# Kernel tuning notes

Hardware: AMD Instinct MI355X
Metric: run time of the kernel (lower is better)

## Reference

```python
import jax, jax.numpy as jnp
import numpy as np

B, S, D, H = 4, 2048, 1024, 16
HD = D // H

def setup_inputs() -> dict:
    key = jax.random.key(0)
    ks = jax.random.split(key, 5)
    scale = 1.0 / np.sqrt(D)
    x = jax.random.normal(ks[0], (B, S, D), dtype=jnp.float32)
    Wq = jax.random.uniform(ks[1], (D, D), dtype=jnp.float32, minval=-scale, maxval=scale)
    Wk = jax.random.uniform(ks[2], (D, D), dtype=jnp.float32, minval=-scale, maxval=scale)
    Wv = jax.random.uniform(ks[3], (D, D), dtype=jnp.float32, minval=-scale, maxval=scale)
    Wo = jax.random.uniform(ks[4], (D, D), dtype=jnp.float32, minval=-scale, maxval=scale)
    return {"x": x, "Wq": Wq, "Wk": Wk, "Wv": Wv, "Wo": Wo}

def reference(x, Wq, Wk, Wv, Wo):
    # q/k/v: [B,S,D] @ [D,D] -> [B,S,H,HD] -> [B,H,S,HD]
    def heads(w):
        return (x @ w.T).reshape(B, S, H, HD).transpose(0, 2, 1, 3)
    q, k, v = heads(Wq), heads(Wk), heads(Wv)
    scores = jnp.einsum('bhqd,bhkd->bhqk', q, k) / np.sqrt(HD).astype(x.dtype)
    attn = jax.nn.softmax(scores, axis=-1)  # [B,H,S,S]
    out = jnp.einsum('bhqk,bhkd->bhqd', attn, v)
    out = out.transpose(0, 2, 1, 3).reshape(B, S, D)
    return out @ Wo.T
```

## Files before the change

### kernel.cpp

```cpp
#include <hip/hip_runtime.h>

typedef unsigned short u16;
typedef unsigned int u32;
typedef __attribute__((ext_vector_type(8))) __bf16 bf16x8;
typedef __attribute__((ext_vector_type(4))) float f32x4;

#define B_  4
#define S_  2048
#define D_  1024
#define H_  16
#define HD_ 64

#define MFMA __builtin_amdgcn_mfma_f32_16x16x32_bf16


__device__ __forceinline__ u16 f2bf(float f) {
  union { float f; u32 u; } v; v.f = f;
  u32 r = v.u + 0x7fffu + ((v.u >> 16) & 1u);
  return (u16)(r >> 16);
}

__device__ __forceinline__ void gld16(const void* g, void* l) {
  __builtin_amdgcn_global_load_lds((__attribute__((address_space(1))) void*)g,
                                   (__attribute__((address_space(3))) void*)l,
                                   16, 0, 0);
}

__device__ __forceinline__ u32 pack_bf(float lo, float hi) {
  u32 a = __builtin_bit_cast(u32, lo) + 0x8000u;
  u32 b = __builtin_bit_cast(u32, hi) + 0x8000u;
  return __builtin_amdgcn_perm(b, a, 0x07060302u);
}

__global__ __launch_bounds__(256) void cvt_kernel(const float* __restrict__ src,
                                                  u16* __restrict__ dst, int n) {
  int i = (blockIdx.x * 256 + threadIdx.x) * 4;
  if (i + 3 < n) {
    float4 v = *(const float4*)(src + i);
    ushort4 o;
    o.x = f2bf(v.x); o.y = f2bf(v.y); o.z = f2bf(v.z); o.w = f2bf(v.w);
    *(ushort4*)(dst + i) = o;
  }
}

__global__ __launch_bounds__(256) void cvt4_kernel(const float* __restrict__ s0,
                                                   const float* __restrict__ s1,
                                                   const float* __restrict__ s2,
                                                   const float* __restrict__ s3,
                                                   u16* __restrict__ dst) {
  const float* srcs[4] = {s0, s1, s2, s3};
  const float* src = srcs[blockIdx.y];
  u16* d = dst + (size_t)blockIdx.y * (D_ * D_);
  int i = (blockIdx.x * 256 + threadIdx.x) * 4;
  float4 v = *(const float4*)(src + i);
  ushort4 o;
  o.x = f2bf(v.x); o.y = f2bf(v.y); o.z = f2bf(v.z); o.w = f2bf(v.w);
  *(ushort4*)(d + i) = o;
}

__global__ __launch_bounds__(256) void gemm_bt(const u16* __restrict__ A,
                                               const u16* __restrict__ Bm,
                                               u16* __restrict__ Qfp,
                                               u16* __restrict__ Kfp,
                                               u16* __restrict__ Vfp,
                                               float* __restrict__ f32Out,
                                               int mode) {
  __shared__ u16 As[128 * 32];
  __shared__ u16 Bs[128 * 32];
  const int t = threadIdx.x, w = t >> 6, l = t & 63;
  const int lrow = l & 15, quad = l >> 4;
  const int wr = w >> 1, wc = w & 1;
  const int r0 = blockIdx.y * 128, c0 = blockIdx.x * 128;
  const int srow = l >> 2, scol = (l & 3) * 8;

  f32x4 acc[4][4] = {};

  for (int k0 = 0; k0 < 1024; k0 += 32) {
#pragma unroll
    for (int j = 0; j < 2; j++) {
      int rowA = 32 * w + 16 * j + srow;
      gld16(A + (size_t)(r0 + rowA) * 1024 + k0 + scol, &As[(32 * w + 16 * j) * 32]);
      gld16(Bm + (size_t)(c0 + rowA) * 1024 + k0 + scol, &Bs[(32 * w + 16 * j) * 32]);
    }
    __syncthreads();

    bf16x8 af[4], bfr[4];
#pragma unroll
    for (int i = 0; i < 4; i++)
      af[i] = *(const bf16x8*)&As[(64 * wr + 16 * i + lrow) * 32 + 8 * quad];
#pragma unroll
    for (int j = 0; j < 4; j++)
      bfr[j] = *(const bf16x8*)&Bs[(64 * wc + 16 * j + lrow) * 32 + 8 * quad];
#pragma unroll
    for (int i = 0; i < 4; i++)
#pragma unroll
      for (int j = 0; j < 4; j++)
        acc[i][j] = MFMA(af[i], bfr[j], acc[i][j], 0, 0, 0);
    __syncthreads();
  }

  if (mode == 1) {
#pragma unroll
    for (int i = 0; i < 4; i++)
#pragma unroll
      for (int j = 0; j < 4; j++)
#pragma unroll
        for (int rr = 0; rr < 4; rr++) {
          int row = r0 + 64 * wr + 16 * i + 4 * quad + rr;
          int col = c0 + 64 * wc + 16 * j + lrow;
          f32Out[(size_t)row * 1024 + col] = acc[i][j][rr];
        }
    return;
  }

  const int mat = c0 >> 10;
  const int hh = ((c0 & 1023) >> 6) + wc;
  const int bb = r0 >> 11;
  const int S0 = (r0 & 2047) + 64 * wr;
  u16* hb = (mat == 0 ? Qfp : (mat == 1 ? Kfp : Vfp)) +
            (size_t)(bb * 16 + hh) * 131072;

  if (mat < 2) {
    const int c_l = quad * 32 + (lrow & 7);
    const int R16 = S0 >> 4;
#pragma unroll
    for (int i = 0; i < 4; i++)
#pragma unroll
      for (int j = 0; j < 4; j++) {
        int oj = (j >> 1) * 512 + ((2 * j + (lrow >> 3)) & 3) * 128;
        u16* p = hb + (R16 + i) * 1024 + oj + c_l;
#pragma unroll
        for (int rr = 0; rr < 4; rr++) p[rr * 8] = f2bf(acc[i][j][rr]);
      }
  } else {
#pragma unroll
    for (int i = 0; i < 4; i++) {
      int blkr = ((S0 >> 5) + ((4 * i + quad) >> 3)) * 4;
      int lanew = (lrow + 16 * ((2 * i + (quad >> 1)) & 3)) * 8 + 4 * (quad & 1);
#pragma unroll
      for (int j = 0; j < 4; j++) {
        uint2 pw;
        pw.x = pack_bf(acc[i][j][0], acc[i][j][1]);
        pw.y = pack_bf(acc[i][j][2], acc[i][j][3]);
        *(uint2*)(hb + (blkr + j) * 512 + lanew) = pw;
      }
    }
  }
}

__global__ __launch_bounds__(256) void attn_kernel(const u16* __restrict__ Qf,
                                                   const u16* __restrict__ Kf,
                                                   const u16* __restrict__ Vf,
                                                   u16* __restrict__ attnb) {
  __shared__ uint2 Ps[4][2][4][16][4];
  const int t = threadIdx.x, w = t >> 6, l = t & 63;
  const int lrow = l & 15, quad = l >> 4;
  const int f = blockIdx.x;
  const int bh = (f & 7) * 8 + (f >> 7);
  const int qb0 = (f >> 3) & 15;
  const int b = bh >> 4, h = bh & 15;
  const int q0 = qb0 * 128;
  const float C = 0.18033688011f;

  const u16* Qh = Qf + (size_t)bh * 131072;
  const u16* kp = Kf + (size_t)bh * 131072 + l * 8;
  const u16* vp = Vf + (size_t)bh * 131072 + l * 8;

  bf16x8 aq[2][2];
#pragma unroll
  for (int g = 0; g < 2; g++) {
    int qb = qb0 * 8 + 2 * w + g;
#pragma unroll
    for (int st = 0; st < 2; st++)
      aq[g][st] = *(const bf16x8*)(Qh + (qb * 2 + st) * 512 + l * 8);
  }

  float lsum[2] = {0.f, 0.f};
  f32x4 acc[2][4] = {};

  for (int kt = 0; kt < S_ / 64; kt++) {
    bf16x8 kf[2][4], vf[2][4];
#pragma unroll
    for (int st = 0; st < 2; st++)
#pragma unroll
      for (int nb = 0; nb < 4; nb++)
        kf[st][nb] = *(const bf16x8*)(kp + (nb * 2 + st) * 512);
#pragma unroll
    for (int st = 0; st < 2; st++)
#pragma unroll
      for (int nb = 0; nb < 4; nb++)
        vf[st][nb] = *(const bf16x8*)(vp + (st * 4 + nb) * 512);
    kp += 4096;
    vp += 4096;

    f32x4 sc[2][4] = {};
#pragma unroll
    for (int st = 0; st < 2; st++)
#pragma unroll
      for (int nb = 0; nb < 4; nb++) {
        sc[0][nb] = MFMA(kf[st][nb], aq[0][st], sc[0][nb], 0, 0, 0);
        sc[1][nb] = MFMA(kf[st][nb], aq[1][st], sc[1][nb], 0, 0, 0);
      }

#pragma unroll
    for (int g = 0; g < 2; g++)
#pragma unroll
      for (int nb = 0; nb < 4; nb++) {
        float p0 = __builtin_amdgcn_exp2f(sc[g][nb][0] * C);
        float p1 = __builtin_amdgcn_exp2f(sc[g][nb][1] * C);
        float p2 = __builtin_amdgcn_exp2f(sc[g][nb][2] * C);
        float p3 = __builtin_amdgcn_exp2f(sc[g][nb][3] * C);
        lsum[g] += (p0 + p1) + (p2 + p3);
        uint2 pw;
        pw.x = pack_bf(p0, p1);
        pw.y = pack_bf(p2, p3);
        Ps[w][g][nb][lrow][quad] = pw;
      }

    bf16x8 pf[2][2];
#pragma unroll
    for (int g = 0; g < 2; g++)
#pragma unroll
      for (int st = 0; st < 2; st++)
        pf[g][st] = *(const bf16x8*)&Ps[w][g][2 * st + (quad >> 1)][lrow][2 * (quad & 1)];

#pragma unroll
    for (int st = 0; st < 2; st++)
#pragma unroll
      for (int nb = 0; nb < 4; nb++) {
        acc[0][nb] = MFMA(pf[0][st], vf[st][nb], acc[0][nb], 0, 0, 0);
        acc[1][nb] = MFMA(pf[1][st], vf[st][nb], acc[1][nb], 0, 0, 0);
      }
  }

#pragma unroll
  for (int g = 0; g < 2; g++) {
    lsum[g] += __shfl_xor(lsum[g], 16, 64);
    lsum[g] += __shfl_xor(lsum[g], 32, 64);
  }
  float linv[2][4];
#pragma unroll
  for (int g = 0; g < 2; g++)
#pragma unroll
    for (int rr = 0; rr < 4; rr++)
      linv[g][rr] = 1.0f / __shfl(lsum[g], 4 * quad + rr, 64);

#pragma unroll
  for (int g = 0; g < 2; g++)
#pragma unroll
    for (int nb = 0; nb < 4; nb++)
#pragma unroll
      for (int rr = 0; rr < 4; rr++) {
        int q = q0 + 32 * w + 16 * g + 4 * quad + rr;
        int dg = h * HD_ + 16 * nb + lrow;
        attnb[((size_t)b * S_ + q) * (size_t)D_ + dg] = f2bf(acc[g][nb][rr] * linv[g][rr]);
      }
}

extern "C" void kernel_launch(void* const* d_in, const int* in_sizes, int n_in,
                              void* d_out, int out_size, void* d_ws, size_t ws_size,
                              hipStream_t stream) {
  const float* x  = (const float*)d_in[0];
  const float* Wq = (const float*)d_in[1];
  const float* Wk = (const float*)d_in[2];
  const float* Wv = (const float*)d_in[3];
  const float* Wo = (const float*)d_in[4];
  float* out = (float*)d_out;

  const size_t NX = (size_t)B_ * S_ * D_;
  const size_t NW = (size_t)D_ * D_;
  u16* xb    = (u16*)d_ws;
  u16* wall  = xb + NX;
  u16* Qf    = wall + 4 * NW;
  u16* Kf    = Qf + NX;
  u16* Vf    = Kf + NX;
  u16* attnb = Vf + NX;

  cvt_kernel<<<NX / 1024, 256, 0, stream>>>(x, xb, (int)NX);
  cvt4_kernel<<<dim3(NW / 1024, 4), 256, 0, stream>>>(Wq, Wk, Wv, Wo, wall);

  gemm_bt<<<dim3(24, 64), 256, 0, stream>>>(xb, wall, Qf, Kf, Vf, nullptr, 0);

  attn_kernel<<<dim3(1024), 256, 0, stream>>>(Qf, Kf, Vf, attnb);

  gemm_bt<<<dim3(8, 64), 256, 0, stream>>>(attnb, wall + 3 * NW, nullptr, nullptr,
                                           nullptr, out, 1);
}
```

Before: 354.4 us.

## Prefetch next K/V tile in registers and stage Q/K epilogue through LDS

```diff
diff --git a/kernel.cpp b/kernel.cpp
--- a/kernel.cpp
+++ b/kernel.cpp
@@ -121,17 +121,22 @@
             (size_t)(bb * 16 + hh) * 131072;
 
   if (mat < 2) {
-    const int c_l = quad * 32 + (lrow & 7);
+    u16* scr = As + w * 1024;
     const int R16 = S0 >> 4;
 #pragma unroll
-    for (int i = 0; i < 4; i++)
+    for (int i = 0; i < 4; i++) {
 #pragma unroll
       for (int j = 0; j < 4; j++) {
-        int oj = (j >> 1) * 512 + ((2 * j + (lrow >> 3)) & 3) * 128;
-        u16* p = hb + (R16 + i) * 1024 + oj + c_l;
-#pragma unroll
-        for (int rr = 0; rr < 4; rr++) p[rr * 8] = f2bf(acc[i][j][rr]);
-      }
+        int oj = (j >> 1) * 512 + ((2 * j + (lrow >> 3)) & 3) * 128 +
+                 quad * 32 + (lrow & 7);
+#pragma unroll
+        for (int rr = 0; rr < 4; rr++) scr[oj + rr * 8] = f2bf(acc[i][j][rr]);
+      }
+      uint4 o0 = *(const uint4*)(scr + l * 8);
+      uint4 o1 = *(const uint4*)(scr + 512 + l * 8);
+      *(uint4*)(hb + (size_t)(R16 + i) * 1024 + l * 8) = o0;
+      *(uint4*)(hb + (size_t)(R16 + i) * 1024 + 512 + l * 8) = o1;
+    }
   } else {
 #pragma unroll
     for (int i = 0; i < 4; i++) {
@@ -148,10 +153,10 @@
   }
 }
 
-__global__ __launch_bounds__(256) void attn_kernel(const u16* __restrict__ Qf,
-                                                   const u16* __restrict__ Kf,
-                                                   const u16* __restrict__ Vf,
-                                                   u16* __restrict__ attnb) {
+__global__ __launch_bounds__(256, 2) void attn_kernel(const u16* __restrict__ Qf,
+                                                      const u16* __restrict__ Kf,
+                                                      const u16* __restrict__ Vf,
+                                                      u16* __restrict__ attnb) {
   __shared__ uint2 Ps[4][2][4][16][4];
   const int t = threadIdx.x, w = t >> 6, l = t & 63;
   const int lrow = l & 15, quad = l >> 4;
@@ -178,28 +183,34 @@
   float lsum[2] = {0.f, 0.f};
   f32x4 acc[2][4] = {};
 
+  bf16x8 kc[2][4], vc[2][4];
+#pragma unroll
+  for (int st = 0; st < 2; st++)
+#pragma unroll
+    for (int nb = 0; nb < 4; nb++) {
+      kc[st][nb] = *(const bf16x8*)(kp + (nb * 2 + st) * 512);
+      vc[st][nb] = *(const bf16x8*)(vp + (st * 4 + nb) * 512);
+    }
+
+#pragma unroll 2
   for (int kt = 0; kt < S_ / 64; kt++) {
-    bf16x8 kf[2][4], vf[2][4];
-#pragma unroll
-    for (int st = 0; st < 2; st++)
-#pragma unroll
-      for (int nb = 0; nb < 4; nb++)
-        kf[st][nb] = *(const bf16x8*)(kp + (nb * 2 + st) * 512);
-#pragma unroll
-    for (int st = 0; st < 2; st++)
-#pragma unroll
-      for (int nb = 0; nb < 4; nb++)
-        vf[st][nb] = *(const bf16x8*)(vp + (st * 4 + nb) * 512);
-    kp += 4096;
-    vp += 4096;
+    kp += 4096; vp += 4096;
+    bf16x8 kn[2][4], vn[2][4];
+#pragma unroll
+    for (int st = 0; st < 2; st++)
+#pragma unroll
+      for (int nb = 0; nb < 4; nb++) {
+        kn[st][nb] = *(const bf16x8*)(kp + (nb * 2 + st) * 512);
+        vn[st][nb] = *(const bf16x8*)(vp + (st * 4 + nb) * 512);
+      }
 
     f32x4 sc[2][4] = {};
 #pragma unroll
     for (int st = 0; st < 2; st++)
 #pragma unroll
       for (int nb = 0; nb < 4; nb++) {
-        sc[0][nb] = MFMA(kf[st][nb], aq[0][st], sc[0][nb], 0, 0, 0);
-        sc[1][nb] = MFMA(kf[st][nb], aq[1][st], sc[1][nb], 0, 0, 0);
+        sc[0][nb] = MFMA(kc[st][nb], aq[0][st], sc[0][nb], 0, 0, 0);
+        sc[1][nb] = MFMA(kc[st][nb], aq[1][st], sc[1][nb], 0, 0, 0);
       }
 
 #pragma unroll
@@ -228,8 +239,16 @@
     for (int st = 0; st < 2; st++)
 #pragma unroll
       for (int nb = 0; nb < 4; nb++) {
-        acc[0][nb] = MFMA(pf[0][st], vf[st][nb], acc[0][nb], 0, 0, 0);
-        acc[1][nb] = MFMA(pf[1][st], vf[st][nb], acc[1][nb], 0, 0, 0);
+        acc[0][nb] = MFMA(pf[0][st], vc[st][nb], acc[0][nb], 0, 0, 0);
+        acc[1][nb] = MFMA(pf[1][st], vc[st][nb], acc[1][nb], 0, 0, 0);
+      }
+
+#pragma unroll
+    for (int st = 0; st < 2; st++)
+#pragma unroll
+      for (int nb = 0; nb < 4; nb++) {
+        kc[st][nb] = kn[st][nb];
+        vc[st][nb] = vn[st][nb];
       }
   }
 
```

Result: faster. 303.5 us (-14.4%).
